# Performance work log

Measured on AMD Instinct MI355X. Metric: run time of the kernel, lower is better.

Reference implementation:

```python
import jax, jax.numpy as jnp
import numpy as np

NZ = 1024       # opts.nz (== NH so layer-0 input weights stack with other layers)
NH = 1024       # opts.nh
NSTATE = 64     # opts.n_state
NLAYERS = 4
MAX_PRIM_LEN = 100
T = MAX_PRIM_LEN + 1   # max_unroll=True runs exactly max_prim_len+1 steps
P_BIAS = 1.0           # opts.dec_p_bias


def setup_inputs() -> dict:
    key = jax.random.key(0)
    ks = jax.random.split(key, 9)
    s_ih = 1.0 / np.sqrt(NH)
    u = lambda k, shape: jax.random.uniform(k, shape, jnp.float32, -s_ih, s_ih)
    return {
        "z": jax.random.normal(ks[0], (1, NZ), jnp.float32),
        # torch LSTM params, gate order (i, f, g, o); layer0 input dim == NZ == NH
        "Wih": u(ks[1], (NLAYERS, 4 * NH, NH)),
        "Whh": u(ks[2], (NLAYERS, 4 * NH, NH)),
        "bih": u(ks[3], (NLAYERS, 4 * NH)),
        "bhh": u(ks[4], (NLAYERS, 4 * NH)),
        "Ws": u(ks[5], (NSTATE, NH)),
        "bs": u(ks[6], (NSTATE,)),
        "Wp": u(ks[7], (2, NH)),
        "bp": u(ks[8], (2,)),
    }


def reference(z, Wih, Whh, bih, bhh, Ws, bs, Wp, bp):
    z0 = z.reshape(-1)  # (NZ,)
    zeros = jnp.zeros_like(z0)

    def step(carry, i):
        h, c = carry                      # each (NLAYERS, NH)
        x = jnp.where(i == 0, z0, zeros)  # input is z at t=0, zeros after
        hs, cs = [], []
        inp = x
        for l in range(NLAYERS):
            gates = Wih[l] @ inp + bih[l] + Whh[l] @ h[l] + bhh[l]
            gi, gf, gg, go = jnp.split(gates, 4)
            cl = jax.nn.sigmoid(gf) * c[l] + jax.nn.sigmoid(gi) * jnp.tanh(gg)
            hl = jax.nn.sigmoid(go) * jnp.tanh(cl)
            hs.append(hl)
            cs.append(cl)
            inp = hl
        o = inp                            # top-layer output, (NH,)
        s = Ws @ o + bs                    # state head, (NSTATE,)
        logits = (Wp @ o + bp).at[0].add(P_BIAS)
        p = jax.nn.softmax(logits)         # (2,)
        last = i == T - 1                  # torch: t > max_prim_len -> force [0,1]
        p = jnp.where(last, jnp.array([0.0, 1.0], p.dtype), p)
        samp = jnp.where(last, 1, 0).astype(jnp.int64)  # max_unroll forces 0 until last
        return (jnp.stack(hs), jnp.stack(cs)), (s, p, samp)

    h0 = jnp.zeros((NLAYERS, NH), z.dtype)
    _, (states, probs, samples) = jax.lax.scan(step, (h0, h0), jnp.arange(T))
    return states[:, None, :], probs[:, None, :], samples[:, None]
```

## Files before the change

### kernel.cpp

```cpp
#include <hip/hip_runtime.h>


#define TT    101
#define NBLK  256
#define NTH   512
#define NREP  8
#define SLAB_U32 512
#define HB16_BYTES (4 * TT * NREP * SLAB_U32 * 4)
#define OUT_PROBS 6464
#define OUT_SAMP  6666
#define SENT 0xFFFFFFFFu

typedef _Float16 h2 __attribute__((ext_vector_type(2)));

__device__ __forceinline__ h2 mkh2(float a, float b) {
    h2 r; r.x = (_Float16)a; r.y = (_Float16)b; return r;
}
__device__ __forceinline__ unsigned pack2(float a, float b) {
    return __builtin_bit_cast(unsigned, mkh2(a, b));
}
__device__ __forceinline__ h2 as_h2(unsigned u) { return __builtin_bit_cast(h2, u); }

#if __has_builtin(__builtin_amdgcn_fdot2)
__device__ __forceinline__ float fdot2(h2 a, h2 b, float c) {
    return __builtin_amdgcn_fdot2(a, b, c, false);
}
#else
__device__ __forceinline__ float fdot2(h2 a, h2 b, float c) {
    return fmaf((float)a.x, (float)b.x, fmaf((float)a.y, (float)b.y, c));
}
#endif

__device__ __forceinline__ uint4 load16_bypass(const uint4* p) {
    uint4 r;
    asm volatile("global_load_dwordx4 %0, %1, off sc0 sc1\n\ts_waitcnt vmcnt(0)"
                 : "=v"(r) : "v"(p) : "memory");
    return r;
}
__device__ __forceinline__ void store4_bypass(unsigned* p, unsigned v) {
    asm volatile("global_store_dword %0, %1, off sc0 sc1" :: "v"(p), "v"(v) : "memory");
}
__device__ __forceinline__ void load32_bypass2(const uint4* p0, const uint4* p1,
                                               uint4& r0, uint4& r1) {
    asm volatile("global_load_dwordx4 %0, %2, off sc0 sc1\n\t"
                 "global_load_dwordx4 %1, %3, off sc0 sc1\n\t"
                 "s_waitcnt vmcnt(0)"
                 : "=&v"(r0), "=&v"(r1) : "v"(p0), "v"(p1) : "memory");
}
__device__ __forceinline__ uint4 poll16(const uint4* p) {
    uint4 r = load16_bypass(p);
    while (r.x == SENT || r.y == SENT || r.z == SENT || r.w == SENT) {
        __builtin_amdgcn_s_sleep(1);
        r = load16_bypass(p);
    }
    return r;
}
__device__ __forceinline__ bool stale(const uint4& u) {
    return (u.x == SENT) | (u.y == SENT) | (u.z == SENT) | (u.w == SENT);
}

__device__ __forceinline__ float wave_sum(float x) {
    int v;
    v = __builtin_amdgcn_update_dpp(0, __builtin_bit_cast(int, x), 0x111, 0xf, 0xf, false);
    x += __builtin_bit_cast(float, v);
    v = __builtin_amdgcn_update_dpp(0, __builtin_bit_cast(int, x), 0x112, 0xf, 0xf, false);
    x += __builtin_bit_cast(float, v);
    v = __builtin_amdgcn_update_dpp(0, __builtin_bit_cast(int, x), 0x114, 0xf, 0xe, false);
    x += __builtin_bit_cast(float, v);
    v = __builtin_amdgcn_update_dpp(0, __builtin_bit_cast(int, x), 0x118, 0xf, 0xc, false);
    x += __builtin_bit_cast(float, v);
    v = __builtin_amdgcn_update_dpp(0, __builtin_bit_cast(int, x), 0x142, 0xa, 0xf, false);
    x += __builtin_bit_cast(float, v);
    v = __builtin_amdgcn_update_dpp(0, __builtin_bit_cast(int, x), 0x143, 0xc, 0xf, false);
    x += __builtin_bit_cast(float, v);
    return __builtin_bit_cast(float, __builtin_amdgcn_readlane(__builtin_bit_cast(int, x), 63));
}

__device__ __forceinline__ float sigm(float x)   { return 1.f / (1.f + __expf(-x)); }
__device__ __forceinline__ float tanh_f(float x) { return 1.f - 2.f / (1.f + __expf(x + x)); }

__global__ __launch_bounds__(NTH, 2) void lstm_kernel(
    const float* __restrict__ z,
    const float* __restrict__ Wih, const float* __restrict__ Whh,
    const float* __restrict__ bih, const float* __restrict__ bhh,
    const float* __restrict__ Ws,  const float* __restrict__ bs,
    const float* __restrict__ Wp,  const float* __restrict__ bp,
    unsigned* __restrict__ hb16, float* __restrict__ out)
{
    const int tid  = threadIdx.x;
    const int wv   = tid >> 6;
    const int lane = tid & 63;
    const int l    = blockIdx.x >> 6;
    const int gb   = blockIdx.x & 63;
    const int uA   = (gb << 4) + (wv << 1);

    __shared__ __align__(16) uint4 vh4[256];
    __shared__ unsigned hout[8];

    h2 w[8][16];
    #pragma unroll
    for (int r = 0; r < 8; ++r) {
        const int u = uA + (r >> 2);
        const int g = r & 3;
        const size_t row = ((size_t)((l << 12) + (g << 10) + u)) << 10;
        const float4* pa = (const float4*)(Whh + row + (lane << 3));
        const float4* pb = (const float4*)(Whh + row + 512 + (lane << 3));
        const float4* pc = (const float4*)(Wih + row + (lane << 3));
        const float4* pd = (const float4*)(Wih + row + 512 + (lane << 3));
        float4 f;
        f = pa[0]; w[r][0]  = mkh2(f.x, f.y); w[r][1]  = mkh2(f.z, f.w);
        f = pa[1]; w[r][2]  = mkh2(f.x, f.y); w[r][3]  = mkh2(f.z, f.w);
        f = pb[0]; w[r][4]  = mkh2(f.x, f.y); w[r][5]  = mkh2(f.z, f.w);
        f = pb[1]; w[r][6]  = mkh2(f.x, f.y); w[r][7]  = mkh2(f.z, f.w);
        f = pc[0]; w[r][8]  = mkh2(f.x, f.y); w[r][9]  = mkh2(f.z, f.w);
        f = pc[1]; w[r][10] = mkh2(f.x, f.y); w[r][11] = mkh2(f.z, f.w);
        f = pd[0]; w[r][12] = mkh2(f.x, f.y); w[r][13] = mkh2(f.z, f.w);
        f = pd[1]; w[r][14] = mkh2(f.x, f.y); w[r][15] = mkh2(f.z, f.w);
    }

    float bA[4], bB[4];
    #pragma unroll
    for (int g = 0; g < 4; ++g) {
        const int iA = (l << 12) + (g << 10) + uA;
        bA[g] = bih[iA] + bhh[iA];
        bB[g] = bih[iA + 1] + bhh[iA + 1];
    }

    const bool role_states = (l == 0 && wv == 6);
    const bool role_probs  = (l == 1 && gb == 0 && wv == 6);
    float hw0[16], hw1[16], hb0 = 0.f, hb1 = 0.f;
    if (role_states) {
        #pragma unroll
        for (int k = 0; k < 16; ++k) hw0[k] = Ws[(gb << 10) + (lane << 4) + k];
        hb0 = bs[gb];
    } else if (role_probs) {
        #pragma unroll
        for (int k = 0; k < 16; ++k) {
            hw0[k] = Wp[(lane << 4) + k];
            hw1[k] = Wp[1024 + (lane << 4) + k];
        }
        hb0 = bp[0]; hb1 = bp[1];
    }
    int th = 0;

    float cstA = 0.f, cstB = 0.f;

    if (tid < 8) hout[tid] = SENT;

    #pragma unroll 1
    for (int t = 0; t < TT; ++t) {
        const bool full = (l > 0) || (t == 0);
        const int rep = (gb + wv) & (NREP - 1);

        if (wv < 2) {
            const int c = (wv << 6) + lane;
            if (t == 0) vh4[c] = make_uint4(0, 0, 0, 0);
            else {
                const uint4* slab = (const uint4*)(hb16 + (size_t)((l * TT + t - 1) * NREP + rep) * SLAB_U32);
                vh4[c] = poll16(slab + c);
            }
        } else if (wv < 4) {
            const int c = ((wv - 2) << 6) + lane;
            if (l > 0) {
                const uint4* slab = (const uint4*)(hb16 + (size_t)(((l - 1) * TT + t) * NREP + rep) * SLAB_U32);
                vh4[128 + c] = poll16(slab + c);
            } else if (t == 0) {
                const float4 f0 = *(const float4*)(z + (c << 3));
                const float4 f1 = *(const float4*)(z + (c << 3) + 4);
                vh4[128 + c] = make_uint4(pack2(f0.x, f0.y), pack2(f0.z, f0.w),
                                          pack2(f1.x, f1.y), pack2(f1.z, f1.w));
            }
        }
        __syncthreads();

        float acc[8] = {0.f, 0.f, 0.f, 0.f, 0.f, 0.f, 0.f, 0.f};
        {
            const uint4 A1 = vh4[lane];
            const uint4 A2 = vh4[64 + lane];
            const unsigned a8[8] = {A1.x, A1.y, A1.z, A1.w, A2.x, A2.y, A2.z, A2.w};
            #pragma unroll
            for (int k = 0; k < 8; ++k) {
                const h2 v2 = as_h2(a8[k]);
                #pragma unroll
                for (int r = 0; r < 8; ++r) acc[r] = fdot2(w[r][k], v2, acc[r]);
            }
            if (full) {
                const uint4 B1 = vh4[128 + lane];
                const uint4 B2 = vh4[192 + lane];
                const unsigned b8[8] = {B1.x, B1.y, B1.z, B1.w, B2.x, B2.y, B2.z, B2.w};
                #pragma unroll
                for (int k = 0; k < 8; ++k) {
                    const h2 v2 = as_h2(b8[k]);
                    #pragma unroll
                    for (int r = 0; r < 8; ++r) acc[r] = fdot2(w[r][8 + k], v2, acc[r]);
                }
            }
        }

        float tot[8];
        #pragma unroll
        for (int r = 0; r < 8; ++r) tot[r] = wave_sum(acc[r]);

        cstA = fmaf(sigm(tot[1] + bA[1]), cstA, sigm(tot[0] + bA[0]) * tanh_f(tot[2] + bA[2]));
        cstB = fmaf(sigm(tot[5] + bB[1]), cstB, sigm(tot[4] + bB[0]) * tanh_f(tot[6] + bB[2]));
        const float hA = sigm(tot[3] + bA[3]) * tanh_f(cstA);
        const float hB = sigm(tot[7] + bB[3]) * tanh_f(cstB);
        if (lane == 0) ((volatile unsigned*)hout)[wv] = pack2(hA, hB);

        if (wv == 7) {
            volatile unsigned* vho = (volatile unsigned*)hout;
            unsigned v = vho[lane & 7];
            while (v == SENT) { v = vho[lane & 7]; }
            unsigned* addr = hb16 + (size_t)(l * TT + t) * NREP * SLAB_U32
                           + (size_t)(lane >> 3) * SLAB_U32 + (gb << 3) + (lane & 7);
            store4_bypass(addr, v);
            if (lane < 8) vho[lane] = SENT;
        } else if ((role_states || role_probs) && th < TT && th <= t - 3) {
            const int hrep = (gb + th) & (NREP - 1);
            const uint4* slab3 = (const uint4*)(hb16 + (size_t)((3 * TT + th) * NREP + hrep) * SLAB_U32);
            uint4 r0, r1;
            load32_bypass2(slab3 + (lane << 1), slab3 + (lane << 1) + 1, r0, r1);
            const bool ok = !(stale(r0) | stale(r1));
            if (__ballot(ok) == ~0ull) {
                const unsigned u8[8] = {r0.x, r0.y, r0.z, r0.w, r1.x, r1.y, r1.z, r1.w};
                if (role_states) {
                    float a = 0.f;
                    #pragma unroll
                    for (int j = 0; j < 8; ++j) {
                        const h2 p = as_h2(u8[j]);
                        a = fmaf(hw0[2 * j], (float)p.x, a);
                        a = fmaf(hw0[2 * j + 1], (float)p.y, a);
                    }
                    const float tots = wave_sum(a);
                    if (lane == 0) out[th * 64 + gb] = tots + hb0;
                } else {
                    float a0 = 0.f, a1 = 0.f;
                    #pragma unroll
                    for (int j = 0; j < 8; ++j) {
                        const h2 p = as_h2(u8[j]);
                        a0 = fmaf(hw0[2 * j], (float)p.x, a0); a0 = fmaf(hw0[2 * j + 1], (float)p.y, a0);
                        a1 = fmaf(hw1[2 * j], (float)p.x, a1); a1 = fmaf(hw1[2 * j + 1], (float)p.y, a1);
                    }
                    const float t0 = wave_sum(a0), t1 = wave_sum(a1);
                    if (lane == 0) {
                        float p0, p1;
                        if (th == TT - 1) { p0 = 0.f; p1 = 1.f; }
                        else {
                            const float l0 = t0 + hb0 + 1.0f;
                            const float l1 = t1 + hb1;
                            const float m  = fmaxf(l0, l1);
                            const float e0 = expf(l0 - m), e1 = expf(l1 - m);
                            const float inv = 1.f / (e0 + e1);
                            p0 = e0 * inv; p1 = e1 * inv;
                        }
                        out[OUT_PROBS + 2 * th]     = p0;
                        out[OUT_PROBS + 2 * th + 1] = p1;
                        out[OUT_SAMP + th] = (th == TT - 1) ? 1.0f : 0.0f;
                    }
                }
                ++th;
            }
        }
        __syncthreads();
    }

    if (role_states || role_probs) {
        while (th < TT) {
            const int hrep = (gb + th) & (NREP - 1);
            const uint4* slab3 = (const uint4*)(hb16 + (size_t)((3 * TT + th) * NREP + hrep) * SLAB_U32);
            uint4 r0, r1;
            for (;;) {
                load32_bypass2(slab3 + (lane << 1), slab3 + (lane << 1) + 1, r0, r1);
                if (!(stale(r0) | stale(r1))) break;
                __builtin_amdgcn_s_sleep(1);
            }
            const unsigned u8[8] = {r0.x, r0.y, r0.z, r0.w, r1.x, r1.y, r1.z, r1.w};
            if (role_states) {
                float a = 0.f;
                #pragma unroll
                for (int j = 0; j < 8; ++j) {
                    const h2 p = as_h2(u8[j]);
                    a = fmaf(hw0[2 * j], (float)p.x, a);
                    a = fmaf(hw0[2 * j + 1], (float)p.y, a);
                }
                const float tots = wave_sum(a);
                if (lane == 0) out[th * 64 + gb] = tots + hb0;
            } else {
                float a0 = 0.f, a1 = 0.f;
                #pragma unroll
                for (int j = 0; j < 8; ++j) {
                    const h2 p = as_h2(u8[j]);
                    a0 = fmaf(hw0[2 * j], (float)p.x, a0); a0 = fmaf(hw0[2 * j + 1], (float)p.y, a0);
                    a1 = fmaf(hw1[2 * j], (float)p.x, a1); a1 = fmaf(hw1[2 * j + 1], (float)p.y, a1);
                }
                const float t0 = wave_sum(a0), t1 = wave_sum(a1);
                if (lane == 0) {
                    float p0, p1;
                    if (th == TT - 1) { p0 = 0.f; p1 = 1.f; }
                    else {
                        const float l0 = t0 + hb0 + 1.0f;
                        const float l1 = t1 + hb1;
                        const float m  = fmaxf(l0, l1);
                        const float e0 = expf(l0 - m), e1 = expf(l1 - m);
                        const float inv = 1.f / (e0 + e1);
                        p0 = e0 * inv; p1 = e1 * inv;
                    }
                    out[OUT_PROBS + 2 * th]     = p0;
                    out[OUT_PROBS + 2 * th + 1] = p1;
                    out[OUT_SAMP + th] = (th == TT - 1) ? 1.0f : 0.0f;
                }
            }
            ++th;
        }
    }
}

extern "C" void kernel_launch(void* const* d_in, const int* in_sizes, int n_in,
                              void* d_out, int out_size, void* d_ws, size_t ws_size,
                              hipStream_t stream)
{
    const float* z   = (const float*)d_in[0];
    const float* Wih = (const float*)d_in[1];
    const float* Whh = (const float*)d_in[2];
    const float* bih = (const float*)d_in[3];
    const float* bhh = (const float*)d_in[4];
    const float* Ws  = (const float*)d_in[5];
    const float* bs  = (const float*)d_in[6];
    const float* Wp  = (const float*)d_in[7];
    const float* bp  = (const float*)d_in[8];
    float* out = (float*)d_out;

    unsigned* hb16 = (unsigned*)d_ws;

    hipMemsetAsync(hb16, 0xFF, HB16_BYTES, stream);
    lstm_kernel<<<NBLK, NTH, 0, stream>>>(z, Wih, Whh, bih, bhh,
                                          Ws, bs, Wp, bp, hb16, out);
}
```

Before: 460.4 us.

## Double-buffer LDS input vector and drop trailing per-step barrier

The shared input vector becomes double-buffered by timestep parity, which lets the block drop the second __syncthreads at the end of each step. The hidden-state publish no longer goes through a single writer wave. Waves 4-7 each pair up with one of waves 0-3 and store both of their values to all replicas, spreading the global stores across four waves. This shortens the serial per-step critical path in the recurrent chain, at the cost of more subtle LDS reuse hazards across steps.

```diff
diff --git a/kernel.cpp b/kernel.cpp
--- a/kernel.cpp
+++ b/kernel.cpp
@@ -94,8 +94,8 @@
     const int gb   = blockIdx.x & 63;
     const int uA   = (gb << 4) + (wv << 1);
 
-    __shared__ __align__(16) uint4 vh4[256];
-    __shared__ unsigned hout[8];
+    __shared__ __align__(16) uint4 vh4[2][256];
+    __shared__ unsigned hout[4];
 
     h2 w[8][16];
     #pragma unroll
@@ -145,38 +145,39 @@
 
     float cstA = 0.f, cstB = 0.f;
 
-    if (tid < 8) hout[tid] = SENT;
+    if (tid < 4) hout[tid] = SENT;
 
     #pragma unroll 1
     for (int t = 0; t < TT; ++t) {
         const bool full = (l > 0) || (t == 0);
+        const int rb = t & 1;
         const int rep = (gb + wv) & (NREP - 1);
 
         if (wv < 2) {
             const int c = (wv << 6) + lane;
-            if (t == 0) vh4[c] = make_uint4(0, 0, 0, 0);
+            if (t == 0) vh4[0][c] = make_uint4(0, 0, 0, 0);
             else {
                 const uint4* slab = (const uint4*)(hb16 + (size_t)((l * TT + t - 1) * NREP + rep) * SLAB_U32);
-                vh4[c] = poll16(slab + c);
+                vh4[rb][c] = poll16(slab + c);
             }
         } else if (wv < 4) {
             const int c = ((wv - 2) << 6) + lane;
             if (l > 0) {
                 const uint4* slab = (const uint4*)(hb16 + (size_t)(((l - 1) * TT + t) * NREP + rep) * SLAB_U32);
-                vh4[128 + c] = poll16(slab + c);
+                vh4[rb][128 + c] = poll16(slab + c);
             } else if (t == 0) {
                 const float4 f0 = *(const float4*)(z + (c << 3));
                 const float4 f1 = *(const float4*)(z + (c << 3) + 4);
-                vh4[128 + c] = make_uint4(pack2(f0.x, f0.y), pack2(f0.z, f0.w),
-                                          pack2(f1.x, f1.y), pack2(f1.z, f1.w));
+                vh4[0][128 + c] = make_uint4(pack2(f0.x, f0.y), pack2(f0.z, f0.w),
+                                             pack2(f1.x, f1.y), pack2(f1.z, f1.w));
             }
         }
         __syncthreads();
 
         float acc[8] = {0.f, 0.f, 0.f, 0.f, 0.f, 0.f, 0.f, 0.f};
         {
-            const uint4 A1 = vh4[lane];
-            const uint4 A2 = vh4[64 + lane];
+            const uint4 A1 = vh4[rb][lane];
+            const uint4 A2 = vh4[rb][64 + lane];
             const unsigned a8[8] = {A1.x, A1.y, A1.z, A1.w, A2.x, A2.y, A2.z, A2.w};
             #pragma unroll
             for (int k = 0; k < 8; ++k) {
@@ -185,8 +186,8 @@
                 for (int r = 0; r < 8; ++r) acc[r] = fdot2(w[r][k], v2, acc[r]);
             }
             if (full) {
-                const uint4 B1 = vh4[128 + lane];
-                const uint4 B2 = vh4[192 + lane];
+                const uint4 B1 = vh4[rb][128 + lane];
+                const uint4 B2 = vh4[rb][192 + lane];
                 const unsigned b8[8] = {B1.x, B1.y, B1.z, B1.w, B2.x, B2.y, B2.z, B2.w};
                 #pragma unroll
                 for (int k = 0; k < 8; ++k) {
@@ -205,17 +206,25 @@
         cstB = fmaf(sigm(tot[5] + bB[1]), cstB, sigm(tot[4] + bB[0]) * tanh_f(tot[6] + bB[2]));
         const float hA = sigm(tot[3] + bA[3]) * tanh_f(cstA);
         const float hB = sigm(tot[7] + bB[3]) * tanh_f(cstB);
-        if (lane == 0) ((volatile unsigned*)hout)[wv] = pack2(hA, hB);
-
-        if (wv == 7) {
+        const unsigned val = pack2(hA, hB);
+
+        if (wv < 4) {
+            if (lane == 0) ((volatile unsigned*)hout)[wv] = val;
+        } else {
             volatile unsigned* vho = (volatile unsigned*)hout;
-            unsigned v = vho[lane & 7];
-            while (v == SENT) { v = vho[lane & 7]; }
-            unsigned* addr = hb16 + (size_t)(l * TT + t) * NREP * SLAB_U32
-                           + (size_t)(lane >> 3) * SLAB_U32 + (gb << 3) + (lane & 7);
-            store4_bypass(addr, v);
-            if (lane < 8) vho[lane] = SENT;
-        } else if ((role_states || role_probs) && th < TT && th <= t - 3) {
+            unsigned bv = vho[wv - 4];
+            while (bv == SENT) { bv = vho[wv - 4]; }
+            if (lane == 0) vho[wv - 4] = SENT;
+            if (lane < 16) {
+                const unsigned sval = (lane < 8) ? val : bv;
+                const int dw = (lane < 8) ? wv : (wv - 4);
+                unsigned* addr = hb16 + (size_t)(l * TT + t) * NREP * SLAB_U32
+                               + (size_t)(lane & 7) * SLAB_U32 + (gb << 3) + dw;
+                store4_bypass(addr, sval);
+            }
+        }
+
+        if ((role_states || role_probs) && th < TT && th <= t - 3) {
             const int hrep = (gb + th) & (NREP - 1);
             const uint4* slab3 = (const uint4*)(hb16 + (size_t)((3 * TT + th) * NREP + hrep) * SLAB_U32);
             uint4 r0, r1;
@@ -261,7 +270,6 @@
                 ++th;
             }
         }
-        __syncthreads();
     }
 
     if (role_states || role_probs) {
```

After: 550.6 us. 1.2x slower.
